# Kernel optimization log

Hardware: AMD Instinct MI355X
Metric: run time of the kernel (lower is better)

## Reference

```python
import jax, jax.numpy as jnp
import numpy as np

B, N, C, H = 32, 577, 768, 12
D = C // H  # head dim 64
HID = 3072  # hardcoded Mlp hidden
ALPHA = 0.1
EPS = 1e-6


def setup_inputs() -> dict:
    key = jax.random.key(0)
    ks = jax.random.split(key, 8)
    s = 0.02
    return {
        "x": jax.random.normal(ks[0], (B, N, C), jnp.float32),
        "attn_weight": jax.random.uniform(ks[1], (B, N - 1), jnp.float32),
        "ln1_w": jnp.ones((C,), jnp.float32),
        "ln1_b": jnp.zeros((C,), jnp.float32),
        "qkv_w": jax.random.normal(ks[2], (3 * C, C), jnp.float32) * s,
        "qkv_b": jnp.zeros((3 * C,), jnp.float32),
        "proj_w": jax.random.normal(ks[3], (C, C), jnp.float32) * s,
        "proj_b": jnp.zeros((C,), jnp.float32),
        "ln2_w": jnp.ones((C,), jnp.float32),
        "ln2_b": jnp.zeros((C,), jnp.float32),
        "fc1_w": jax.random.normal(ks[4], (HID, C), jnp.float32) * s,
        "fc1_b": jnp.zeros((HID,), jnp.float32),
        "fc2_w": jax.random.normal(ks[5], (C, HID), jnp.float32) * s,
        "fc2_b": jnp.zeros((C,), jnp.float32),
    }


def _ln(x, w, b):
    m = x.mean(-1, keepdims=True)
    v = jnp.var(x, axis=-1, keepdims=True)
    return (x - m) * jax.lax.rsqrt(v + EPS) * w + b


def reference(x, attn_weight, ln1_w, ln1_b, qkv_w, qkv_b, proj_w, proj_b,
              ln2_w, ln2_b, fc1_w, fc1_b, fc2_w, fc2_b):
    h = _ln(x, ln1_w, ln1_b)
    qkv = (h @ qkv_w.T + qkv_b).reshape(B, N, 3, H, D)
    q = qkv[:, :, 0].transpose(0, 2, 1, 3)  # [B,H,N,D]
    k = qkv[:, :, 1].transpose(0, 2, 1, 3)
    v = qkv[:, :, 2].transpose(0, 2, 1, 3)
    scale = D ** -0.5
    attn = jnp.einsum('bhnd,bhmd->bhnm', q, k) * scale  # [B,H,N,N]
    patch_attn = attn[:, :, 0, 1:]  # pre-reweight CLS->patch scores
    # multiplicative reweighting of CLS row (cols 1:) before softmax
    factor = jnp.concatenate(
        [jnp.ones((B, 1), attn.dtype), attn_weight * ALPHA + (1.0 - ALPHA)], axis=-1)
    attn = attn.at[:, :, 0, :].multiply(factor[:, None, :])
    attn = jax.nn.softmax(attn, axis=-1)
    out = jnp.einsum('bhnm,bhmd->bhnd', attn, v)
    out = out.transpose(0, 2, 1, 3).reshape(B, N, C)
    out = out @ proj_w.T + proj_b
    x = x + out
    h2 = _ln(x, ln2_w, ln2_b)
    h2 = jax.nn.gelu(h2 @ fc1_w.T + fc1_b, approximate=False)  # nn.GELU exact
    h2 = h2 @ fc2_w.T + fc2_b
    x = x + h2
    return (x, patch_attn)
```

## Files before the change

kernel.cpp:

```cpp
#include <hip/hip_runtime.h>
#include <hip/hip_bf16.h>
#include <cstdint>

#define BB 32
#define NN 577
#define CC 768
#define HH 12
#define HIDN 3072
#define MROWS (BB*NN)

typedef __attribute__((ext_vector_type(8))) short bf16x8;
typedef __attribute__((ext_vector_type(4))) float f32x4;

__device__ __forceinline__ float b2f(unsigned short u) {
    union { float f; unsigned int i; } x; x.i = ((unsigned int)u) << 16; return x.f;
}
__device__ __forceinline__ unsigned short f2b(float f) {
    union { float f; unsigned int i; } x; x.f = f;
    unsigned int i = x.i;
    i += 0x7fffu + ((i >> 16) & 1u);
    return (unsigned short)(i >> 16);
}

__device__ __forceinline__ void async16(const void* g, void* l) {
    __builtin_amdgcn_global_load_lds(
        (const __attribute__((address_space(1))) uint32_t*)g,
        (__attribute__((address_space(3))) uint32_t*)l, 16, 0, 0);
}

__device__ __forceinline__ float gelu_f(float v) {
    float ax = fabsf(v) * 0.70710678118654752f;
    float t = __builtin_amdgcn_rcpf(1.0f + 0.3275911f * ax);
    float poly = t * (0.254829592f + t * (-0.284496736f + t * (1.421413741f +
                 t * (-1.453152027f + t * 1.061405429f))));
    float e = __expf(-ax * ax);
    float erf_abs = 1.0f - poly * e;
    float erf_v = (v >= 0.f) ? erf_abs : -erf_abs;
    return 0.5f * v * (1.0f + erf_v);
}

__global__ void cvt4(const float* __restrict__ a, int na, unsigned short* __restrict__ oa,
                     const float* __restrict__ b, int nb, unsigned short* __restrict__ ob,
                     const float* __restrict__ c, int nc, unsigned short* __restrict__ oc,
                     const float* __restrict__ d, int nd, unsigned short* __restrict__ od) {
    int stride = gridDim.x * blockDim.x;
    int t = blockIdx.x * blockDim.x + threadIdx.x;
    for (int i = t; i < na; i += stride) oa[i] = f2b(a[i]);
    for (int i = t; i < nb; i += stride) ob[i] = f2b(b[i]);
    for (int i = t; i < nc; i += stride) oc[i] = f2b(c[i]);
    for (int i = t; i < nd; i += stride) od[i] = f2b(d[i]);
}

__global__ __launch_bounds__(256)
void ln_kernel(const float* __restrict__ x, const float* __restrict__ w,
               const float* __restrict__ bsv, unsigned short* __restrict__ out) {
    int row = blockIdx.x;
    const float* xr = x + (size_t)row * CC;
    float v[3]; float s = 0.f, ss = 0.f;
    #pragma unroll
    for (int i = 0; i < 3; ++i) {
        v[i] = xr[threadIdx.x + i * 256];
        s += v[i]; ss += v[i] * v[i];
    }
    int lane = threadIdx.x & 63, wv = threadIdx.x >> 6;
    #pragma unroll
    for (int off = 32; off; off >>= 1) { s += __shfl_down(s, off); ss += __shfl_down(ss, off); }
    __shared__ float rs[4], rss[4];
    __shared__ float mean_s, rstd_s;
    if (lane == 0) { rs[wv] = s; rss[wv] = ss; }
    __syncthreads();
    if (threadIdx.x == 0) {
        float S = rs[0] + rs[1] + rs[2] + rs[3];
        float SS = rss[0] + rss[1] + rss[2] + rss[3];
        float m = S * (1.0f / 768.0f);
        float var = SS * (1.0f / 768.0f) - m * m;
        mean_s = m; rstd_s = rsqrtf(var + 1e-6f);
    }
    __syncthreads();
    float m = mean_s, r = rstd_s;
    #pragma unroll
    for (int i = 0; i < 3; ++i) {
        int c = threadIdx.x + i * 256;
        out[(size_t)row * CC + c] = f2b((v[i] - m) * r * w[c] + bsv[c]);
    }
}

template <int EPI>
__global__ __launch_bounds__(256)
void gemm_bt(const unsigned short* __restrict__ A, const unsigned short* __restrict__ Bw,
             const float* __restrict__ bias, const float* __restrict__ resid,
             unsigned short* __restrict__ outb, float* __restrict__ outf,
             int M, int N, int K) {
    const int NT = gridDim.x;
    const int MT = (M + 127) >> 7;
    int flat = blockIdx.y * NT + blockIdx.x;
    int xcd = flat & 7, s = flat >> 3;
    int n_t = s % NT, mj = s / NT;
    int m_t = xcd + 8 * mj;
    if (m_t >= MT) return;
    const int m0 = m_t * 128, n0 = n_t * 128;

    __shared__ __align__(16) unsigned short As[2][128 * 32];
    __shared__ __align__(16) unsigned short Bs[2][128 * 32];
    const int tid = threadIdx.x;
    const int wave = tid >> 6, lane = tid & 63;
    const int wr = wave >> 1, wc = wave & 1;
    const int quad = lane >> 4, l16 = lane & 15;

    f32x4 acc[4][4] = {};

    const int c0 = tid, c1 = 256 + tid;
    const int row0 = c0 >> 2, seg0 = c0 & 3;
    const int row1 = c1 >> 2, seg1 = c1 & 3;
    int gm0 = m0 + row0; if (gm0 > M - 1) gm0 = M - 1;
    int gm1 = m0 + row1; if (gm1 > M - 1) gm1 = M - 1;
    const unsigned short* a0 = A + (size_t)gm0 * K + seg0 * 8;
    const unsigned short* a1 = A + (size_t)gm1 * K + seg1 * 8;
    const unsigned short* b0 = Bw + (size_t)(n0 + row0) * K + seg0 * 8;
    const unsigned short* b1 = Bw + (size_t)(n0 + row1) * K + seg1 * 8;

    for (int k0 = 0; k0 < K; k0 += 64) {
        #pragma unroll
        for (int p = 0; p < 2; ++p) {
            int kk = k0 + p * 32;
            async16(a0 + kk, &As[p][c0 * 8]);
            async16(a1 + kk, &As[p][c1 * 8]);
            async16(b0 + kk, &Bs[p][c0 * 8]);
            async16(b1 + kk, &Bs[p][c1 * 8]);
        }
        __syncthreads();
        #pragma unroll
        for (int p = 0; p < 2; ++p) {
            bf16x8 af[4], bfr[4];
            #pragma unroll
            for (int mi = 0; mi < 4; ++mi)
                af[mi] = *(const bf16x8*)&As[p][(wr * 64 + mi * 16 + l16) * 32 + quad * 8];
            #pragma unroll
            for (int ni = 0; ni < 4; ++ni)
                bfr[ni] = *(const bf16x8*)&Bs[p][(wc * 64 + ni * 16 + l16) * 32 + quad * 8];
            #pragma unroll
            for (int mi = 0; mi < 4; ++mi)
                #pragma unroll
                for (int ni = 0; ni < 4; ++ni)
                    acc[mi][ni] = __builtin_amdgcn_mfma_f32_16x16x32_bf16(af[mi], bfr[ni], acc[mi][ni], 0, 0, 0);
        }
        __syncthreads();
    }

    #pragma unroll
    for (int mi = 0; mi < 4; ++mi) {
        #pragma unroll
        for (int r = 0; r < 4; ++r) {
            int grow = m0 + wr * 64 + mi * 16 + quad * 4 + r;
            if (grow >= M) continue;
            #pragma unroll
            for (int ni = 0; ni < 4; ++ni) {
                int gcol = n0 + wc * 64 + ni * 16 + l16;
                float v = acc[mi][ni][r] + bias[gcol];
                size_t idx = (size_t)grow * N + gcol;
                if (EPI == 0) {
                    outb[idx] = f2b(v);
                } else if (EPI == 1) {
                    outb[idx] = f2b(gelu_f(v));
                } else {
                    outf[idx] = resid[idx] + v;
                }
            }
        }
    }
}

__global__ __launch_bounds__(256)
void attn_mfma(const unsigned short* __restrict__ qkv, const float* __restrict__ aw,
               unsigned short* __restrict__ O, float* __restrict__ patch) {
    const int qt = blockIdx.x, h = blockIdx.y, b = blockIdx.z;
    const int tid = threadIdx.x, wv = tid >> 6, lane = tid & 63;
    const int quad = lane >> 4, l16 = lane & 15;

    __shared__ __align__(16) unsigned short Ks[64 * 72];
    __shared__ __align__(16) unsigned short Vt[64 * 72];
    __shared__ __align__(16) unsigned short Pt[4][64 * 18];
    __shared__ __align__(16) float Sw[4][16 * 68];

    int qrow = qt * 64 + wv * 16 + l16;
    int qclamp = qrow < NN ? qrow : NN - 1;
    const unsigned short* qbase = qkv + (size_t)(b * NN + qclamp) * 2304 + h * 64;
    bf16x8 qf[2];
    qf[0] = *(const bf16x8*)(qbase + quad * 8);
    qf[1] = *(const bf16x8*)(qbase + 32 + quad * 8);

    f32x4 o[4] = {};
    float mst = -1.0e30f;
    float lst = 0.f;

    for (int kt = 0; kt < 10; ++kt) {
        __syncthreads();
        #pragma unroll
        for (int i = 0; i < 2; ++i) {
            int c = i * 256 + tid;
            int key = c >> 3, seg = c & 7;
            int gk = kt * 64 + key; if (gk >= NN) gk = NN - 1;
            const unsigned short* kb = qkv + (size_t)(b * NN + gk) * 2304 + 768 + h * 64 + seg * 8;
            bf16x8 kv = *(const bf16x8*)kb;
            *(bf16x8*)&Ks[key * 72 + seg * 8] = kv;
            const unsigned short* vb = qkv + (size_t)(b * NN + gk) * 2304 + 1536 + h * 64 + seg * 8;
            bf16x8 vvv = *(const bf16x8*)vb;
            int kg = key >> 3, kl = key & 7;
            int swz = (kg ^ seg) * 8 + kl;
            #pragma unroll
            for (int e = 0; e < 8; ++e)
                Vt[(seg * 8 + e) * 72 + swz] = ((const unsigned short*)&vvv)[e];
        }
        __syncthreads();

        f32x4 s[4];
        #pragma unroll
        for (int ni = 0; ni < 4; ++ni) {
            bf16x8 b0 = *(const bf16x8*)&Ks[(ni * 16 + l16) * 72 + quad * 8];
            bf16x8 b1 = *(const bf16x8*)&Ks[(ni * 16 + l16) * 72 + 32 + quad * 8];
            f32x4 acc = {};
            acc = __builtin_amdgcn_mfma_f32_16x16x32_bf16(qf[0], b0, acc, 0, 0, 0);
            acc = __builtin_amdgcn_mfma_f32_16x16x32_bf16(qf[1], b1, acc, 0, 0, 0);
            s[ni] = acc;
        }

        float* SwW = Sw[wv];
        #pragma unroll
        for (int ni = 0; ni < 4; ++ni)
            #pragma unroll
            for (int r = 0; r < 4; ++r)
                SwW[(quad * 4 + r) * 68 + ni * 16 + l16] = s[ni][r] * 0.125f;

        if (kt == 9) {
            #pragma unroll
            for (int j = 0; j < 16; ++j) {
                int gkey = kt * 64 + quad * 16 + j;
                if (gkey >= NN) SwW[l16 * 68 + quad * 16 + j] = -1.0e30f;
            }
        }

        if (qt == 0 && wv == 0 && l16 == 0) {
            #pragma unroll
            for (int j = 0; j < 16; ++j) {
                int gkey = kt * 64 + quad * 16 + j;
                if (gkey >= 1 && gkey < NN) {
                    float v = SwW[0 * 68 + quad * 16 + j];
                    patch[(size_t)(b * HH + h) * (NN - 1) + gkey - 1] = v;
                    float f = aw[b * (NN - 1) + gkey - 1] * 0.1f + 0.9f;
                    SwW[0 * 68 + quad * 16 + j] = v * f;
                }
            }
        }

        const float* Srow = &SwW[l16 * 68];
        float tm = -1.0e30f;
        #pragma unroll
        for (int j = 0; j < 16; ++j) tm = fmaxf(tm, Srow[quad * 16 + j]);
        tm = fmaxf(tm, __shfl_xor(tm, 16));
        tm = fmaxf(tm, __shfl_xor(tm, 32));
        float nm = fmaxf(mst, tm);
        float alpha = __expf(mst - nm);
        mst = nm;
        float rsum = 0.f;
        #pragma unroll
        for (int j = 0; j < 16; ++j) {
            float p = __expf(Srow[quad * 16 + j] - nm);
            Pt[wv][(quad * 16 + j) * 18 + l16] = f2b(p);
            rsum += p;
        }
        rsum += __shfl_xor(rsum, 16);
        rsum += __shfl_xor(rsum, 32);
        lst = lst * alpha + rsum;

        #pragma unroll
        for (int r = 0; r < 4; ++r) {
            float ar = __shfl(alpha, quad * 4 + r);
            #pragma unroll
            for (int ni = 0; ni < 4; ++ni) o[ni][r] *= ar;
        }

        #pragma unroll
        for (int kc = 0; kc < 2; ++kc) {
            union { bf16x8 v; unsigned short u[8]; } af;
            #pragma unroll
            for (int j = 0; j < 8; ++j)
                af.u[j] = Pt[wv][(kc * 32 + quad * 8 + j) * 18 + l16];
            #pragma unroll
            for (int ni = 0; ni < 4; ++ni) {
                int d = ni * 16 + l16;
                int gs = (kc * 4 + quad) ^ (d >> 3);
                bf16x8 vf = *(const bf16x8*)&Vt[d * 72 + gs * 8];
                o[ni] = __builtin_amdgcn_mfma_f32_16x16x32_bf16(af.v, vf, o[ni], 0, 0, 0);
            }
        }
    }

    #pragma unroll
    for (int r = 0; r < 4; ++r) {
        float lr = __shfl(lst, quad * 4 + r);
        float inv = (lr > 0.f) ? __builtin_amdgcn_rcpf(lr) : 0.f;
        int row = qt * 64 + wv * 16 + quad * 4 + r;
        if (row < NN) {
            #pragma unroll
            for (int ni = 0; ni < 4; ++ni)
                O[(size_t)(b * NN + row) * CC + h * 64 + ni * 16 + l16] = f2b(o[ni][r] * inv);
        }
    }
}

extern "C" void kernel_launch(void* const* d_in, const int* in_sizes, int n_in,
                              void* d_out, int out_size, void* d_ws, size_t ws_size,
                              hipStream_t stream) {
    const float* x       = (const float*)d_in[0];
    const float* aw      = (const float*)d_in[1];
    const float* ln1w    = (const float*)d_in[2];
    const float* ln1b    = (const float*)d_in[3];
    const float* qkvw_f  = (const float*)d_in[4];
    const float* qkvb    = (const float*)d_in[5];
    const float* projw_f = (const float*)d_in[6];
    const float* projb   = (const float*)d_in[7];
    const float* ln2w    = (const float*)d_in[8];
    const float* ln2b    = (const float*)d_in[9];
    const float* fc1w_f  = (const float*)d_in[10];
    const float* fc1b    = (const float*)d_in[11];
    const float* fc2w_f  = (const float*)d_in[12];
    const float* fc2b    = (const float*)d_in[13];

    char* ws = (char*)d_ws;
    unsigned short* h_bf  = (unsigned short*)(ws + 0);
    unsigned short* qkv   = (unsigned short*)(ws + 28360704);
    unsigned short* g1    = (unsigned short*)(ws + 0);
    unsigned short* attno = (unsigned short*)(ws + 113442816);
    float*          x1    = (float*)(ws + 141803520);
    unsigned short* h2    = (unsigned short*)(ws + 198524928);
    unsigned short* qkvw  = (unsigned short*)(ws + 226885632);
    unsigned short* projw = (unsigned short*)(ws + 230424576);
    unsigned short* fc1w  = (unsigned short*)(ws + 231604224);
    unsigned short* fc2w  = (unsigned short*)(ws + 236322816);

    float* out_x = (float*)d_out;
    float* out_patch = out_x + (size_t)MROWS * CC;

    cvt4<<<1024, 256, 0, stream>>>(qkvw_f, 2304 * 768, qkvw,
                                   projw_f, 768 * 768, projw,
                                   fc1w_f, 3072 * 768, fc1w,
                                   fc2w_f, 768 * 3072, fc2w);
    ln_kernel<<<MROWS, 256, 0, stream>>>(x, ln1w, ln1b, h_bf);
    gemm_bt<0><<<dim3(18, 152), 256, 0, stream>>>(h_bf, qkvw, qkvb, nullptr, qkv, nullptr,
                                                  MROWS, 2304, 768);
    attn_mfma<<<dim3(10, HH, BB), 256, 0, stream>>>(qkv, aw, attno, out_patch);
    gemm_bt<2><<<dim3(6, 152), 256, 0, stream>>>(attno, projw, projb, x, nullptr, x1,
                                                 MROWS, 768, 768);
    ln_kernel<<<MROWS, 256, 0, stream>>>(x1, ln2w, ln2b, h2);
    gemm_bt<1><<<dim3(24, 152), 256, 0, stream>>>(h2, fc1w, fc1b, nullptr, g1, nullptr,
                                                  MROWS, 3072, 768);
    gemm_bt<2><<<dim3(6, 152), 256, 0, stream>>>(g1, fc2w, fc2b, x1, nullptr, out_x,
                                                 MROWS, 768, 3072);
}
```

Baseline: 787.2 us.

## Keep attention softmax in registers instead of staging scores through LDS

The attention kernel no longer writes the QK^T scores to a shared-memory buffer and reads them back for the online softmax. Row max and row sum are now computed directly on the MFMA accumulator layout, using 16-lane xor shuffles and per-row running statistics. The scaled P tile is written to LDS row-major, so it can be loaded as a single bf16x8 vector for the PV MFMA. The 1/8 scale is folded into Q at load time, which is exact in bf16 because it is a power of two. The cost is more register pressure from the four per-row max and sum values, plus extra shuffles.

```diff
diff --git a/kernel.cpp b/kernel.cpp
--- a/kernel.cpp
+++ b/kernel.cpp
@@ -179,8 +179,7 @@
 
     __shared__ __align__(16) unsigned short Ks[64 * 72];
     __shared__ __align__(16) unsigned short Vt[64 * 72];
-    __shared__ __align__(16) unsigned short Pt[4][64 * 18];
-    __shared__ __align__(16) float Sw[4][16 * 68];
+    __shared__ __align__(16) unsigned short Pt[4][16 * 72];
 
     int qrow = qt * 64 + wv * 16 + l16;
     int qclamp = qrow < NN ? qrow : NN - 1;
@@ -188,10 +187,18 @@
     bf16x8 qf[2];
     qf[0] = *(const bf16x8*)(qbase + quad * 8);
     qf[1] = *(const bf16x8*)(qbase + 32 + quad * 8);
+    #pragma unroll
+    for (int i = 0; i < 2; ++i) {
+        union { bf16x8 v; unsigned short u[8]; } t; t.v = qf[i];
+        #pragma unroll
+        for (int j = 0; j < 8; ++j) t.u[j] = f2b(b2f(t.u[j]) * 0.125f);
+        qf[i] = t.v;
+    }
 
     f32x4 o[4] = {};
-    float mst = -1.0e30f;
-    float lst = 0.f;
+    float mst[4], lst[4];
+    #pragma unroll
+    for (int r = 0; r < 4; ++r) { mst[r] = -1.0e30f; lst[r] = 0.f; }
 
     for (int kt = 0; kt < 10; ++kt) {
         __syncthreads();
@@ -224,81 +231,74 @@
             s[ni] = acc;
         }
 
-        float* SwW = Sw[wv];
-        #pragma unroll
-        for (int ni = 0; ni < 4; ++ni)
-            #pragma unroll
-            for (int r = 0; r < 4; ++r)
-                SwW[(quad * 4 + r) * 68 + ni * 16 + l16] = s[ni][r] * 0.125f;
-
         if (kt == 9) {
             #pragma unroll
-            for (int j = 0; j < 16; ++j) {
-                int gkey = kt * 64 + quad * 16 + j;
-                if (gkey >= NN) SwW[l16 * 68 + quad * 16 + j] = -1.0e30f;
-            }
-        }
-
-        if (qt == 0 && wv == 0 && l16 == 0) {
-            #pragma unroll
-            for (int j = 0; j < 16; ++j) {
-                int gkey = kt * 64 + quad * 16 + j;
+            for (int ni = 0; ni < 4; ++ni) {
+                if (ni * 16 + l16 != 0) {
+                    #pragma unroll
+                    for (int r = 0; r < 4; ++r) s[ni][r] = -1.0e30f;
+                }
+            }
+        }
+
+        if (qt == 0 && wv == 0 && quad == 0) {
+            #pragma unroll
+            for (int ni = 0; ni < 4; ++ni) {
+                int gkey = kt * 64 + ni * 16 + l16;
                 if (gkey >= 1 && gkey < NN) {
-                    float v = SwW[0 * 68 + quad * 16 + j];
-                    patch[(size_t)(b * HH + h) * (NN - 1) + gkey - 1] = v;
+                    patch[(size_t)(b * HH + h) * (NN - 1) + gkey - 1] = s[ni][0];
                     float f = aw[b * (NN - 1) + gkey - 1] * 0.1f + 0.9f;
-                    SwW[0 * 68 + quad * 16 + j] = v * f;
+                    s[ni][0] *= f;
                 }
             }
         }
 
-        const float* Srow = &SwW[l16 * 68];
-        float tm = -1.0e30f;
-        #pragma unroll
-        for (int j = 0; j < 16; ++j) tm = fmaxf(tm, Srow[quad * 16 + j]);
-        tm = fmaxf(tm, __shfl_xor(tm, 16));
-        tm = fmaxf(tm, __shfl_xor(tm, 32));
-        float nm = fmaxf(mst, tm);
-        float alpha = __expf(mst - nm);
-        mst = nm;
-        float rsum = 0.f;
-        #pragma unroll
-        for (int j = 0; j < 16; ++j) {
-            float p = __expf(Srow[quad * 16 + j] - nm);
-            Pt[wv][(quad * 16 + j) * 18 + l16] = f2b(p);
-            rsum += p;
-        }
-        rsum += __shfl_xor(rsum, 16);
-        rsum += __shfl_xor(rsum, 32);
-        lst = lst * alpha + rsum;
-
+        float al[4];
         #pragma unroll
         for (int r = 0; r < 4; ++r) {
-            float ar = __shfl(alpha, quad * 4 + r);
-            #pragma unroll
-            for (int ni = 0; ni < 4; ++ni) o[ni][r] *= ar;
+            float tm = fmaxf(fmaxf(s[0][r], s[1][r]), fmaxf(s[2][r], s[3][r]));
+            tm = fmaxf(tm, __shfl_xor(tm, 1));
+            tm = fmaxf(tm, __shfl_xor(tm, 2));
+            tm = fmaxf(tm, __shfl_xor(tm, 4));
+            tm = fmaxf(tm, __shfl_xor(tm, 8));
+            float nm = fmaxf(mst[r], tm);
+            al[r] = __expf(mst[r] - nm);
+            mst[r] = nm;
+        }
+        #pragma unroll
+        for (int r = 0; r < 4; ++r) {
+            float rs = 0.f;
+            #pragma unroll
+            for (int ni = 0; ni < 4; ++ni) {
+                float p = __expf(s[ni][r] - mst[r]);
+                Pt[wv][(quad * 4 + r) * 72 + ni * 16 + l16] = f2b(p);
+                rs += p;
+            }
+            rs += __shfl_xor(rs, 1);
+            rs += __shfl_xor(rs, 2);
+            rs += __shfl_xor(rs, 4);
+            rs += __shfl_xor(rs, 8);
+            lst[r] = lst[r] * al[r] + rs;
+            #pragma unroll
+            for (int ni = 0; ni < 4; ++ni) o[ni][r] *= al[r];
         }
 
         #pragma unroll
         for (int kc = 0; kc < 2; ++kc) {
-            union { bf16x8 v; unsigned short u[8]; } af;
-            #pragma unroll
-            for (int j = 0; j < 8; ++j)
-                af.u[j] = Pt[wv][(kc * 32 + quad * 8 + j) * 18 + l16];
+            bf16x8 af = *(const bf16x8*)&Pt[wv][l16 * 72 + kc * 32 + quad * 8];
             #pragma unroll
             for (int ni = 0; ni < 4; ++ni) {
                 int d = ni * 16 + l16;
                 int gs = (kc * 4 + quad) ^ (d >> 3);
                 bf16x8 vf = *(const bf16x8*)&Vt[d * 72 + gs * 8];
-                o[ni] = __builtin_amdgcn_mfma_f32_16x16x32_bf16(af.v, vf, o[ni], 0, 0, 0);
+                o[ni] = __builtin_amdgcn_mfma_f32_16x16x32_bf16(af, vf, o[ni], 0, 0, 0);
             }
         }
     }
 
     #pragma unroll
     for (int r = 0; r < 4; ++r) {
-        float lr = __shfl(lst, quad * 4 + r);
-        float inv = (lr > 0.f) ? __builtin_amdgcn_rcpf(lr) : 0.f;
+        float inv = (lst[r] > 0.f) ? __builtin_amdgcn_rcpf(lst[r]) : 0.f;
         int row = qt * 64 + wv * 16 + quad * 4 + r;
         if (row < NN) {
             #pragma unroll
```

New measurement: 752.1 us. 1.05x faster.
